# Kernel optimization log

Measured on AMD Instinct MI355X. Metric: run time of the kernel, lower is better.

Reference implementation:

```python
import jax, jax.numpy as jnp
import numpy as np
from jax import lax

ALPHA = 0.95
THETA = 1.0
GAMMA = 12.0
GAIN = 1.0  # gain buffer value used in forward (detached in torch via .item())
KERNELS = (8, 16, 32)
B, T = 256, 16384


@jax.custom_vjp
def surrogate_spike(x):
    # forward: hard threshold at 0
    return (x >= 0).astype(x.dtype)


def _spike_fwd(x):
    return surrogate_spike(x), x


def _spike_bwd(x, g):
    ax = jnp.abs(GAMMA * x)
    grad = (ax < 1.0).astype(x.dtype) * (1.0 - ax) * GAMMA
    return (g * grad,)


surrogate_spike.defvjp(_spike_fwd, _spike_bwd)


def causal_conv(x, w):
    # x: [B,1,T], w: [1,1,k] -> [B,T]; left-pad k-1 (causal), cross-correlation like torch Conv1d
    k = w.shape[-1]
    out = lax.conv_general_dilated(
        x, w, window_strides=(1,), padding=[(k - 1, 0)],
        dimension_numbers=("NCH", "OIH", "NCH"))
    return out[:, 0, :]


def lif_wta(u):
    # u: [B,K,T] -> spikes s_all [B,K,T]
    Bb, K, Tt = u.shape

    def step(v, u_t):  # v,u_t: [B,K]
        v = ALPHA * v + u_t
        m = v - THETA
        s_raw = surrogate_spike(m)
        mask = jax.nn.one_hot(jnp.argmax(m, axis=1), K, dtype=m.dtype)  # top-1 WTA
        s = s_raw * mask
        return v - s * THETA, s

    v0 = jnp.zeros((Bb, K), u.dtype)
    _, s_all = lax.scan(step, v0, jnp.moveaxis(u, 2, 0))  # [T,B,K]
    return jnp.moveaxis(s_all, 0, 2)  # [B,K,T]


def setup_inputs() -> dict:
    key = jax.random.key(0)
    kx, k0, k1, k2, ky = jax.random.split(key, 5)
    x = jax.random.normal(kx, (B, 1, T), dtype=jnp.float32)
    w0 = jax.random.normal(k0, (1, 1, 8), dtype=jnp.float32) / np.sqrt(8.0)
    w1 = jax.random.normal(k1, (1, 1, 16), dtype=jnp.float32) / np.sqrt(16.0)
    w2 = jax.random.normal(k2, (1, 1, 32), dtype=jnp.float32) / np.sqrt(32.0)
    y = jax.random.randint(ky, (B, T), 0, 2, dtype=jnp.int32)
    return {"x": x, "w0": w0, "w1": w1, "w2": w2, "y": y}


def reference(x, w0, w1, w2, y):
    ws = (w0, w1, w2)
    # per-branch causal conv, scaled by 1/sqrt(k), then gain
    u = jnp.stack(
        [causal_conv(x, w) * (1.0 / np.sqrt(float(k))) for w, k in zip(ws, KERNELS)],
        axis=1) * GAIN  # [B,K,T]
    s_all = lif_wta(u)
    return (u, s_all)
```

## Files before the change

### kernel.cpp

```cpp
#include <hip/hip_runtime.h>
#include <math.h>

constexpr int B = 256;
constexpr int T = 16384;
constexpr int K = 3;

constexpr int CHUNK = 256;
constexpr int WARM  = 512;

constexpr int CBT = 128;
constexpr int CWT = 32;


__global__ __launch_bounds__(256, 2) void conv_kernel(
    const float* __restrict__ x,
    const float* __restrict__ w0f,
    const float* __restrict__ w1f,
    const float* __restrict__ w2f,
    float*  __restrict__ u_out,
    double* __restrict__ w64)
{
    const int blk = blockIdx.x;
    const int bgi = blk >> 7;
    const int t0  = (blk & 127) * CBT;
    const int b0  = bgi * 64;
    const int tid = threadIdx.x;

    __shared__ float sx[64][164];
    for (int k = tid; k < 64 * 40; k += 256) {
        const int r  = k / 40;
        const int c4 = k - r * 40;
        const int g  = t0 - 32 + 4 * c4;
        float4 v = make_float4(0.f, 0.f, 0.f, 0.f);
        if (g >= 0) v = *(const float4*)(x + (size_t)(b0 + r) * T + g);
        *(float4*)&sx[r][4 * c4] = v;
    }
    __syncthreads();

    const int lane    = tid & 63;
    const int w       = tid >> 6;
    const int t_start = t0 + CWT * w;

    double w0d[8], w1d[16], w2d[32];
#pragma unroll
    for (int i = 0; i < 8; ++i)  w0d[i] = (double)w0f[i];
#pragma unroll
    for (int i = 0; i < 16; ++i) w1d[i] = (double)w1f[i];
#pragma unroll
    for (int i = 0; i < 32; ++i) w2d[i] = (double)w2f[i];

    double win[32];
#pragma unroll
    for (int k = 1; k < 32; ++k) win[k] = (double)sx[lane][CWT * w + k];

    const double s8  = 1.0 / sqrt(8.0);
    const double s32 = 1.0 / sqrt(32.0);

    float fr0[16], fr1[16], fr2[16];
    float* uf = u_out + (size_t)(b0 + lane) * (3 * T);

#pragma unroll
    for (int j = 0; j < CWT; ++j) {
        win[j & 31] = (double)sx[lane][CWT * w + 32 + j];
        double a0 = 0.0, a1 = 0.0, a2 = 0.0;
#pragma unroll
        for (int i = 0; i < 8; ++i)  a0 = fma(w0d[i], win[(j + 25 + i) & 31], a0);
#pragma unroll
        for (int i = 0; i < 16; ++i) a1 = fma(w1d[i], win[(j + 17 + i) & 31], a1);
#pragma unroll
        for (int i = 0; i < 32; ++i) a2 = fma(w2d[i], win[(j + 1 + i) & 31], a2);
        a0 *= s8; a1 *= 0.25; a2 *= s32;

        const int t = t_start + j;
        double* wp = w64 + ((size_t)(t >> 4) * 4 + bgi) * 3072 + (size_t)lane * 2;
        const int D0 = (j & 15) * 3;
        wp[((D0    ) >> 1) * 128 + ((D0    ) & 1)] = a0 - 0.05;
        wp[((D0 + 1) >> 1) * 128 + ((D0 + 1) & 1)] = a1 - 0.05;
        wp[((D0 + 2) >> 1) * 128 + ((D0 + 2) & 1)] = a2 - 0.05;

        fr0[j & 15] = (float)a0; fr1[j & 15] = (float)a1; fr2[j & 15] = (float)a2;
        if ((j & 15) == 15) {
            float* d = uf + t_start + (j & ~15);
#pragma unroll
            for (int q = 0; q < 4; ++q) {
                *(float4*)(d + 4 * q)         = ((float4*)fr0)[q];
                *(float4*)(d + T + 4 * q)     = ((float4*)fr1)[q];
                *(float4*)(d + 2 * T + 4 * q) = ((float4*)fr2)[q];
            }
        }
    }
}

__global__ __launch_bounds__(64, 1) void scan_kernel(
    const double* __restrict__ w64,
    float* __restrict__ s_out)
{
    const int c  = blockIdx.x & 63;
    const int bg = blockIdx.x >> 6;
    const int i  = threadIdx.x;
    const int chain = bg * 64 + i;

    const int t_emit = c * CHUNK;
    const int t_w    = (t_emit >= WARM) ? (t_emit - WARM) : 0;
    const int warm_g = (t_emit - t_w) >> 4;
    const int n_g    = warm_g + (CHUNK >> 4);
    const int tw16   = t_w >> 4;

    float* sb = s_out + (size_t)chain * (3 * T);

    double m0 = -1.0, m1 = -1.0, m2 = -1.0;
    double cA[48], cB[48], cC[48];

#define LOADG(dst, gg) do {                                                   \
    const double2* _s =                                                       \
        (const double2*)(w64 + ((size_t)(tw16 + (gg)) * 4 + bg) * 3072) + i;  \
    _Pragma("unroll")                                                         \
    for (int _q = 0; _q < 24; ++_q)                                           \
        ((double2*)(dst))[_q] = _s[(size_t)_q * 64];                          \
} while (0)

#define STEP(W0, W1, W2, O0, O1, O2) do {                               \
    const double M0 = fma(0.95, m0, (W0));                              \
    const double M1 = fma(0.95, m1, (W1));                              \
    const double M2 = fma(0.95, m2, (W2));                              \
    const bool c01 = (M0 >= M1);                                        \
    const bool c02 = (M0 >= M2);                                        \
    const bool c12 = (M1 >= M2);                                        \
    const bool f0  = (M0 >= 0.0);                                       \
    const bool f1  = (M1 >= 0.0);                                       \
    const bool f2  = (M2 >= 0.0);                                       \
    const bool s0 = c01 & c02 & f0;             \
    const bool s1 = (!c01) & c12 & f1;                                  \
    const bool s2 = (!c02) & (!c12) & f2;                               \
    m0 = s0 ? M0 - 1.0 : M0;                                            \
    m1 = s1 ? M1 - 1.0 : M1;                                            \
    m2 = s2 ? M2 - 1.0 : M2;                                            \
    (O0) = s0 ? 1.0f : 0.0f;                                            \
    (O1) = s1 ? 1.0f : 0.0f;                                            \
    (O2) = s2 ? 1.0f : 0.0f;                                            \
} while (0)

#define PHASE(buf, gg) do {                                             \
    if ((gg) < n_g) {                                                   \
        float sp0[16], sp1[16], sp2[16];                                \
        _Pragma("unroll")                                               \
        for (int _j = 0; _j < 16; ++_j)                                 \
            STEP((buf)[3*_j], (buf)[3*_j+1], (buf)[3*_j+2],             \
                 sp0[_j], sp1[_j], sp2[_j]);                            \
        if ((gg) >= warm_g) {                                           \
            float* _d = sb + t_w + (size_t)(gg) * 16;                   \
            _Pragma("unroll")                                           \
            for (int _q = 0; _q < 4; ++_q) {                            \
                *(float4*)(_d + 4*_q)         = ((float4*)sp0)[_q];     \
                *(float4*)(_d + T + 4*_q)     = ((float4*)sp1)[_q];     \
                *(float4*)(_d + 2*T + 4*_q)   = ((float4*)sp2)[_q];     \
            }                                                           \
        }                                                               \
        if ((gg) + 3 < n_g) LOADG(buf, (gg) + 3);                       \
    }                                                                   \
} while (0)

    LOADG(cA, 0);
    LOADG(cB, 1);
    LOADG(cC, 2);
    for (int g = 0; g < n_g; g += 3) {
        PHASE(cA, g);
        PHASE(cB, g + 1);
        PHASE(cC, g + 2);
    }

#undef PHASE
#undef STEP
#undef LOADG
}

extern "C" void kernel_launch(void* const* d_in, const int* in_sizes, int n_in,
                              void* d_out, int out_size, void* d_ws, size_t ws_size,
                              hipStream_t stream)
{
    const float* x  = (const float*)d_in[0];
    const float* w0 = (const float*)d_in[1];
    const float* w1 = (const float*)d_in[2];
    const float* w2 = (const float*)d_in[3];

    float* out   = (float*)d_out;
    float* u_out = out;
    float* s_out = out + (size_t)B * K * T;

    double* w64 = (double*)d_ws;

    conv_kernel<<<(B / 64) * (T / CBT), 256, 0, stream>>>(x, w0, w1, w2, u_out, w64);
    scan_kernel<<<B, 64, 0, stream>>>(w64, s_out);
}
```

Baseline: 241.4 us.

## Stream scan inputs via global_load_lds into triple-buffered LDS ring

Replaces the scan kernel's register-file triple buffer (three 48-double arrays per lane) with direct global-to-LDS asynchronous loads into a shared-memory ring of three stages. Waits use hand-tuned vmcnt thresholds that depend on whether each step group emits stores. This is meant to free the 144 doubles of register pressure and let the loads overlap the serial recurrence. The risks are fragile hand-computed vmcnt counts, which may be wrong in edge cases such as the first chunk with no warmup, plus added LDS read latency inside the dependent chain.

Measured after the change: 246.7 us. +2.2%, slower.

```diff
diff --git a/kernel.cpp b/kernel.cpp
--- a/kernel.cpp
+++ b/kernel.cpp
@@ -95,10 +95,10 @@
     const double* __restrict__ w64,
     float* __restrict__ s_out)
 {
-    const int c  = blockIdx.x & 63;
-    const int bg = blockIdx.x >> 6;
-    const int i  = threadIdx.x;
-    const int chain = bg * 64 + i;
+    const int c    = blockIdx.x & 63;
+    const int bg   = blockIdx.x >> 6;
+    const int lane = threadIdx.x;
+    const int chain = bg * 64 + lane;
 
     const int t_emit = c * CHUNK;
     const int t_w    = (t_emit >= WARM) ? (t_emit - WARM) : 0;
@@ -108,15 +108,23 @@
 
     float* sb = s_out + (size_t)chain * (3 * T);
 
+    __shared__ double2 lbuf[3 * 1536];
+
     double m0 = -1.0, m1 = -1.0, m2 = -1.0;
-    double cA[48], cB[48], cC[48];
-
-#define LOADG(dst, gg) do {                                                   \
-    const double2* _s =                                                       \
-        (const double2*)(w64 + ((size_t)(tw16 + (gg)) * 4 + bg) * 3072) + i;  \
+
+#define WAITN(N) asm volatile("s_waitcnt vmcnt(" #N ")" ::: "memory")
+
+#define LOADDMA(s, gg) do {                                                   \
+    const double2* _src = (const double2*)(w64 +                              \
+        ((size_t)(tw16 + (gg)) * 4 + bg) * 3072) + lane;                      \
     _Pragma("unroll")                                                         \
     for (int _q = 0; _q < 24; ++_q)                                           \
-        ((double2*)(dst))[_q] = _s[(size_t)_q * 64];                          \
+        __builtin_amdgcn_global_load_lds(                                     \
+            (const __attribute__((address_space(1))) void*)(const void*)      \
+                (_src + (size_t)_q * 64),                                     \
+            (__attribute__((address_space(3))) void*)(void*)                  \
+                (&lbuf[(s) * 1536 + _q * 64]),                                \
+            16, 0, 0);                                                        \
 } while (0)
 
 #define STEP(W0, W1, W2, O0, O1, O2) do {                               \
@@ -140,38 +148,55 @@
     (O2) = s2 ? 1.0f : 0.0f;                                            \
 } while (0)
 
-#define PHASE(buf, gg) do {                                             \
-    if ((gg) < n_g) {                                                   \
-        float sp0[16], sp1[16], sp2[16];                                \
-        _Pragma("unroll")                                               \
-        for (int _j = 0; _j < 16; ++_j)                                 \
-            STEP((buf)[3*_j], (buf)[3*_j+1], (buf)[3*_j+2],             \
-                 sp0[_j], sp1[_j], sp2[_j]);                            \
-        if ((gg) >= warm_g) {                                           \
-            float* _d = sb + t_w + (size_t)(gg) * 16;                   \
-            _Pragma("unroll")                                           \
-            for (int _q = 0; _q < 4; ++_q) {                            \
-                *(float4*)(_d + 4*_q)         = ((float4*)sp0)[_q];     \
-                *(float4*)(_d + T + 4*_q)     = ((float4*)sp1)[_q];     \
-                *(float4*)(_d + 2*T + 4*_q)   = ((float4*)sp2)[_q];     \
-            }                                                           \
-        }                                                               \
-        if ((gg) + 3 < n_g) LOADG(buf, (gg) + 3);                       \
-    }                                                                   \
+#define BODY(s, pp) do {                                                      \
+    if ((pp) < n_g) {                                                         \
+        if ((pp) == n_g - 1)            WAITN(24);                            \
+        else if ((pp) == n_g - 2)       WAITN(48);                            \
+        else if ((pp) >= warm_g + 2)    WAITN(63);                            \
+        else if ((pp) == warm_g + 1)    WAITN(60);                            \
+        else                            WAITN(48);                            \
+        const double* _lp = (const double*)(lbuf + (s) * 1536) + 2 * lane;    \
+        float sp0[16], sp1[16], sp2[16];                                      \
+        _Pragma("unroll")                                                     \
+        for (int _j = 0; _j < 16; ++_j) {                                     \
+            const int _d0 = 3 * _j;                                           \
+            const double _W0 = _lp[((_d0    ) >> 1) * 128 + ((_d0    ) & 1)]; \
+            const double _W1 = _lp[((_d0 + 1) >> 1) * 128 + ((_d0 + 1) & 1)]; \
+            const double _W2 = _lp[((_d0 + 2) >> 1) * 128 + ((_d0 + 2) & 1)]; \
+            STEP(_W0, _W1, _W2, sp0[_j], sp1[_j], sp2[_j]);                   \
+        }                                                                     \
+        if ((pp) >= warm_g) {                                                 \
+            float* _d = sb + t_w + (size_t)(pp) * 16;                         \
+            _Pragma("unroll")                                                 \
+            for (int _q = 0; _q < 4; ++_q) {                                  \
+                *(float4*)(_d + 4*_q)         = ((float4*)sp0)[_q];           \
+                *(float4*)(_d + T + 4*_q)     = ((float4*)sp1)[_q];           \
+                *(float4*)(_d + 2*T + 4*_q)   = ((float4*)sp2)[_q];           \
+            }                                                                 \
+        }                                                                     \
+        if ((pp) + 3 < n_g) {                                                 \
+            \
+            \
+            \
+            asm volatile("s_waitcnt lgkmcnt(0)" ::: "memory");                \
+            LOADDMA(s, (pp) + 3);                                             \
+        }                                                                     \
+    }                                                                         \
 } while (0)
 
-    LOADG(cA, 0);
-    LOADG(cB, 1);
-    LOADG(cC, 2);
-    for (int g = 0; g < n_g; g += 3) {
-        PHASE(cA, g);
-        PHASE(cB, g + 1);
-        PHASE(cC, g + 2);
+    LOADDMA(0, 0);
+    LOADDMA(1, 1);
+    LOADDMA(2, 2);
+    for (int p = 0; p < n_g; p += 3) {
+        BODY(0, p);
+        BODY(1, p + 1);
+        BODY(2, p + 2);
     }
 
-#undef PHASE
+#undef BODY
 #undef STEP
-#undef LOADG
+#undef LOADDMA
+#undef WAITN
 }
 
 extern "C" void kernel_launch(void* const* d_in, const int* in_sizes, int n_in,
```

## Fuse causal conv into chunked LIF scan, recomputing conv during warmup

Applied to the files above, without the earlier changes.

Replaces the separate conv kernel and the double-precision workspace round trip with one kernel. Each 64-lane block owns 64 chains for one 64-step chunk, recomputes the conv over its 512-step warmup region, feeds the values straight into the WTA scan, and writes u and spikes through an LDS transpose as coalesced float4 stores. Chunks are mapped to XCDs by block index. This removes the workspace write and read traffic, but with chunk 64 and warmup 512 every block does about nine times its own share of conv and scan work, and each block holds only one wave.

Measured after the change: 323.6 us. 34.0% more time.

```diff
diff --git a/kernel.cpp b/kernel.cpp
--- a/kernel.cpp
+++ b/kernel.cpp
@@ -5,41 +5,34 @@
 constexpr int T = 16384;
 constexpr int K = 3;
 
-constexpr int CHUNK = 256;
+constexpr int CHUNK = 64;
 constexpr int WARM  = 512;
 
-constexpr int CBT = 128;
-constexpr int CWT = 32;
+#define XCOMP(v, jj) ( ((jj) & 3) == 0 ? (v).x                          \
+                     : ((jj) & 3) == 1 ? (v).y                          \
+                     : ((jj) & 3) == 2 ? (v).z : (v).w )
 
-
-__global__ __launch_bounds__(256, 2) void conv_kernel(
+__global__ __launch_bounds__(64, 1) void fused_kernel(
     const float* __restrict__ x,
     const float* __restrict__ w0f,
     const float* __restrict__ w1f,
     const float* __restrict__ w2f,
-    float*  __restrict__ u_out,
-    double* __restrict__ w64)
+    float* __restrict__ u_out,
+    float* __restrict__ s_out)
 {
-    const int blk = blockIdx.x;
-    const int bgi = blk >> 7;
-    const int t0  = (blk & 127) * CBT;
-    const int b0  = bgi * 64;
-    const int tid = threadIdx.x;
+    const int phys = blockIdx.x;
+    const int xcd  = phys & 7;
+    const int slot = phys >> 3;
+    const int c    = xcd * 32 + (slot & 31);
+    const int bg   = slot >> 5;
+    const int lane = threadIdx.x;
+    const int chain = bg * 64 + lane;
 
-    __shared__ float sx[64][164];
-    for (int k = tid; k < 64 * 40; k += 256) {
-        const int r  = k / 40;
-        const int c4 = k - r * 40;
-        const int g  = t0 - 32 + 4 * c4;
-        float4 v = make_float4(0.f, 0.f, 0.f, 0.f);
-        if (g >= 0) v = *(const float4*)(x + (size_t)(b0 + r) * T + g);
-        *(float4*)&sx[r][4 * c4] = v;
-    }
-    __syncthreads();
+    const int t_emit = c * CHUNK;
+    const int t_w    = (t_emit >= WARM) ? (t_emit - WARM) : 0;
+    const int n_g    = ((t_emit + CHUNK) - t_w) >> 4;
 
-    const int lane    = tid & 63;
-    const int w       = tid >> 6;
-    const int t_start = t0 + CWT * w;
+    const float* xc = x + (size_t)chain * T;
 
     double w0d[8], w1d[16], w2d[32];
 #pragma unroll
@@ -49,75 +42,27 @@
 #pragma unroll
     for (int i = 0; i < 32; ++i) w2d[i] = (double)w2f[i];
 
-    double win[32];
-#pragma unroll
-    for (int k = 1; k < 32; ++k) win[k] = (double)sx[lane][CWT * w + k];
-
     const double s8  = 1.0 / sqrt(8.0);
     const double s32 = 1.0 / sqrt(32.0);
 
-    float fr0[16], fr1[16], fr2[16];
-    float* uf = u_out + (size_t)(b0 + lane) * (3 * T);
+    double win[32];
+    win[0] = 0.0;
+#pragma unroll
+    for (int s = 1; s < 32; ++s) {
+        const int t = t_w - 32 + s;
+        win[s] = (t >= 0) ? (double)xc[t] : 0.0;
+    }
 
+    float4 pA[4], pB[4];
 #pragma unroll
-    for (int j = 0; j < CWT; ++j) {
-        win[j & 31] = (double)sx[lane][CWT * w + 32 + j];
-        double a0 = 0.0, a1 = 0.0, a2 = 0.0;
+    for (int q = 0; q < 4; ++q) pA[q] = *(const float4*)(xc + t_w + 4 * q);
 #pragma unroll
-        for (int i = 0; i < 8; ++i)  a0 = fma(w0d[i], win[(j + 25 + i) & 31], a0);
-#pragma unroll
-        for (int i = 0; i < 16; ++i) a1 = fma(w1d[i], win[(j + 17 + i) & 31], a1);
-#pragma unroll
-        for (int i = 0; i < 32; ++i) a2 = fma(w2d[i], win[(j + 1 + i) & 31], a2);
-        a0 *= s8; a1 *= 0.25; a2 *= s32;
+    for (int q = 0; q < 4; ++q) pB[q] = *(const float4*)(xc + t_w + 16 + 4 * q);
 
-        const int t = t_start + j;
-        double* wp = w64 + ((size_t)(t >> 4) * 4 + bgi) * 3072 + (size_t)lane * 2;
-        const int D0 = (j & 15) * 3;
-        wp[((D0    ) >> 1) * 128 + ((D0    ) & 1)] = a0 - 0.05;
-        wp[((D0 + 1) >> 1) * 128 + ((D0 + 1) & 1)] = a1 - 0.05;
-        wp[((D0 + 2) >> 1) * 128 + ((D0 + 2) & 1)] = a2 - 0.05;
-
-        fr0[j & 15] = (float)a0; fr1[j & 15] = (float)a1; fr2[j & 15] = (float)a2;
-        if ((j & 15) == 15) {
-            float* d = uf + t_start + (j & ~15);
-#pragma unroll
-            for (int q = 0; q < 4; ++q) {
-                *(float4*)(d + 4 * q)         = ((float4*)fr0)[q];
-                *(float4*)(d + T + 4 * q)     = ((float4*)fr1)[q];
-                *(float4*)(d + 2 * T + 4 * q) = ((float4*)fr2)[q];
-            }
-        }
-    }
-}
-
-__global__ __launch_bounds__(64, 1) void scan_kernel(
-    const double* __restrict__ w64,
-    float* __restrict__ s_out)
-{
-    const int c  = blockIdx.x & 63;
-    const int bg = blockIdx.x >> 6;
-    const int i  = threadIdx.x;
-    const int chain = bg * 64 + i;
-
-    const int t_emit = c * CHUNK;
-    const int t_w    = (t_emit >= WARM) ? (t_emit - WARM) : 0;
-    const int warm_g = (t_emit - t_w) >> 4;
-    const int n_g    = warm_g + (CHUNK >> 4);
-    const int tw16   = t_w >> 4;
-
-    float* sb = s_out + (size_t)chain * (3 * T);
+    __shared__ float4 ustage[12 * 65];
+    __shared__ float4 sstage[12 * 65];
 
     double m0 = -1.0, m1 = -1.0, m2 = -1.0;
-    double cA[48], cB[48], cC[48];
-
-#define LOADG(dst, gg) do {                                                   \
-    const double2* _s =                                                       \
-        (const double2*)(w64 + ((size_t)(tw16 + (gg)) * 4 + bg) * 3072) + i;  \
-    _Pragma("unroll")                                                         \
-    for (int _q = 0; _q < 24; ++_q)                                           \
-        ((double2*)(dst))[_q] = _s[(size_t)_q * 64];                          \
-} while (0)
 
 #define STEP(W0, W1, W2, O0, O1, O2) do {                               \
     const double M0 = fma(0.95, m0, (W0));                              \
@@ -140,38 +85,78 @@
     (O2) = s2 ? 1.0f : 0.0f;                                            \
 } while (0)
 
-#define PHASE(buf, gg) do {                                             \
-    if ((gg) < n_g) {                                                   \
-        float sp0[16], sp1[16], sp2[16];                                \
-        _Pragma("unroll")                                               \
-        for (int _j = 0; _j < 16; ++_j)                                 \
-            STEP((buf)[3*_j], (buf)[3*_j+1], (buf)[3*_j+2],             \
-                 sp0[_j], sp1[_j], sp2[_j]);                            \
-        if ((gg) >= warm_g) {                                           \
-            float* _d = sb + t_w + (size_t)(gg) * 16;                   \
-            _Pragma("unroll")                                           \
-            for (int _q = 0; _q < 4; ++_q) {                            \
-                *(float4*)(_d + 4*_q)         = ((float4*)sp0)[_q];     \
-                *(float4*)(_d + T + 4*_q)     = ((float4*)sp1)[_q];     \
-                *(float4*)(_d + 2*T + 4*_q)   = ((float4*)sp2)[_q];     \
-            }                                                           \
-        }                                                               \
-        if ((gg) + 3 < n_g) LOADG(buf, (gg) + 3);                       \
-    }                                                                   \
+#define CSTEP(j, TPAR, PC) do {                                               \
+    const float _xf = XCOMP((PC)[(j) >> 2], j);                               \
+    win[((TPAR) + (j)) & 31] = (double)_xf;                                   \
+    double a0 = 0.0, a1 = 0.0, a2 = 0.0;                                      \
+    _Pragma("unroll")                                                         \
+    for (int i = 0; i < 8; ++i)                                               \
+        a0 = fma(w0d[i], win[((TPAR) + (j) + 25 + i) & 31], a0);              \
+    _Pragma("unroll")                                                         \
+    for (int i = 0; i < 16; ++i)                                              \
+        a1 = fma(w1d[i], win[((TPAR) + (j) + 17 + i) & 31], a1);              \
+    _Pragma("unroll")                                                         \
+    for (int i = 0; i < 32; ++i)                                              \
+        a2 = fma(w2d[i], win[((TPAR) + (j) + 1 + i) & 31], a2);               \
+    a0 *= s8; a1 *= 0.25; a2 *= s32;                                          \
+    fr0[j] = (float)a0; fr1[j] = (float)a1; fr2[j] = (float)a2;               \
+    STEP(a0 - 0.05, a1 - 0.05, a2 - 0.05, sp0[j], sp1[j], sp2[j]);            \
 } while (0)
 
-    LOADG(cA, 0);
-    LOADG(cB, 1);
-    LOADG(cC, 2);
-    for (int g = 0; g < n_g; g += 3) {
-        PHASE(cA, g);
-        PHASE(cB, g + 1);
-        PHASE(cC, g + 2);
+#define EMIT(g) do {                                                          \
+    _Pragma("unroll")                                                         \
+    for (int _q = 0; _q < 4; ++_q) {                                          \
+        ustage[(0 * 4 + _q) * 65 + lane] = ((float4*)fr0)[_q];                \
+        ustage[(1 * 4 + _q) * 65 + lane] = ((float4*)fr1)[_q];                \
+        ustage[(2 * 4 + _q) * 65 + lane] = ((float4*)fr2)[_q];                \
+        sstage[(0 * 4 + _q) * 65 + lane] = ((float4*)sp0)[_q];                \
+        sstage[(1 * 4 + _q) * 65 + lane] = ((float4*)sp1)[_q];                \
+        sstage[(2 * 4 + _q) * 65 + lane] = ((float4*)sp2)[_q];                \
+    }                                                                         \
+    asm volatile("s_waitcnt lgkmcnt(0)" ::: "memory");                        \
+    __builtin_amdgcn_sched_barrier(0);                                        \
+    const int _t = t_w + (g) * 16;                                            \
+    _Pragma("unroll")                                                         \
+    for (int _k = 0; _k < 3; ++_k) {                                          \
+        _Pragma("unroll")                                                     \
+        for (int _q = 0; _q < 4; ++_q) {                                      \
+            const int _row = _q * 16 + (lane >> 2);                           \
+            const float4 _vu = ustage[(_k * 4 + (lane & 3)) * 65 + _row];     \
+            const float4 _vs = sstage[(_k * 4 + (lane & 3)) * 65 + _row];     \
+            const size_t _off = (size_t)(bg * 64 + _row) * (3 * T)            \
+                              + (size_t)_k * T + _t + (lane & 3) * 4;         \
+            *(float4*)(u_out + _off) = _vu;                                   \
+            *(float4*)(s_out + _off) = _vs;                                   \
+        }                                                                     \
+    }                                                                         \
+} while (0)
+
+#define GROUP(g, TPAR, PC) do {                                               \
+    if ((g) < n_g) {                                                          \
+        float fr0[16], fr1[16], fr2[16];                                      \
+        float sp0[16], sp1[16], sp2[16];                                      \
+        _Pragma("unroll")                                                     \
+        for (int _j = 0; _j < 16; ++_j) CSTEP(_j, TPAR, PC);                  \
+        if ((g) + 2 < n_g) {                                                  \
+            const float* _pb = xc + t_w + ((g) + 2) * 16;                     \
+            _Pragma("unroll")                                                 \
+            for (int _q = 0; _q < 4; ++_q)                                    \
+                (PC)[_q] = *(const float4*)(_pb + 4 * _q);                    \
+            __builtin_amdgcn_sched_barrier(0);                                \
+        }                                                                     \
+        if ((g) >= n_g - 4) EMIT(g);                                          \
+    }                                                                         \
+} while (0)
+
+    for (int gp = 0; gp < n_g; gp += 2) {
+        GROUP(gp,     0,  pA);
+        GROUP(gp + 1, 16, pB);
     }
 
-#undef PHASE
+#undef GROUP
+#undef EMIT
+#undef CSTEP
 #undef STEP
-#undef LOADG
 }
 
 extern "C" void kernel_launch(void* const* d_in, const int* in_sizes, int n_in,
@@ -186,9 +171,8 @@
     float* out   = (float*)d_out;
     float* u_out = out;
     float* s_out = out + (size_t)B * K * T;
+    (void)d_ws; (void)ws_size;
 
-    double* w64 = (double*)d_ws;
-
-    conv_kernel<<<(B / 64) * (T / CBT), 256, 0, stream>>>(x, w0, w1, w2, u_out, w64);
-    scan_kernel<<<B, 64, 0, stream>>>(w64, s_out);
+    fused_kernel<<<(B / 64) * (T / CHUNK), 64, 0, stream>>>(
+        x, w0, w1, w2, u_out, s_out);
 }
```
